# Performance work log

Measured on AMD Instinct MI355X. Metric: run time of the kernel, lower is better.

## Reference

```python
import jax, jax.numpy as jnp
import numpy as np

B, T, D, N, R, K = 4, 4096, 1024, 64, 16, 4  # batch, seq, d_model, state_size, dt_rank, conv_kernel


def setup_inputs() -> dict:
    key = jax.random.key(0)
    ks = jax.random.split(key, 6)
    s = 0.02  # small init scale (original uses xavier/zeros; random here for a meaningful baseline)
    return {
        "x": jax.random.normal(ks[0], (B, T, D), jnp.float32),
        "conv_w": jax.random.normal(ks[1], (D, K), jnp.float32) * s,  # depthwise conv kernel [D, K]
        "in_w": jax.random.normal(ks[2], (N, D), jnp.float32) * s,    # input_proj weight
        "in_b": jnp.zeros((N,), jnp.float32),
        "dt_w": jax.random.normal(ks[3], (R, D), jnp.float32) * s,    # delta_proj weight
        "dt_b": jnp.zeros((R,), jnp.float32),
        "tr_w": jax.random.normal(ks[4], (N, R), jnp.float32) * s,    # transition weight (no bias)
        "out_w": jax.random.normal(ks[5], (D, N), jnp.float32) * s,   # output_proj weight
        "out_b": jnp.zeros((D,), jnp.float32),
    }


def reference(x, conv_w, in_w, in_b, dt_w, dt_b, tr_w, out_w, out_b):
    Bx, Tx, Dx = x.shape
    k = conv_w.shape[1]
    # Causal depthwise conv: torch Conv1d(pad=k-1, groups=D) then slice [:T]
    xp = jnp.pad(x, ((0, 0), (k - 1, 0), (0, 0)))  # left-pad time axis
    conv_out = sum(xp[:, j:j + Tx, :] * conv_w[:, j] for j in range(k))  # [B,T,D]
    projected = (x + conv_out) @ in_w.T + in_b                 # [B,T,N]
    delta = jnp.tanh(x @ dt_w.T + dt_b) @ tr_w.T               # [B,T,N]

    def step(state, inp):
        d_t, p_t = inp  # each [B,N]
        state = jax.nn.silu(d_t + state) + p_t
        return state, state

    init = jnp.zeros((Bx, in_w.shape[0]), x.dtype)
    _, states = jax.lax.scan(step, init,
                             (jnp.swapaxes(delta, 0, 1), jnp.swapaxes(projected, 0, 1)))
    states = jnp.swapaxes(states, 0, 1)  # [B,T,N]
    return states @ out_w.T + out_b      # [B,T,D] (dropout=0.0 -> identity)
```

## Files before the change

kernel.cpp:

```cpp
#include <hip/hip_runtime.h>
#include <math.h>

#define Bn 4
#define Tn 4096
#define Dn 1024
#define Nn 64
#define Rn 16
#define KCONV 4

#define TT2 32
#define KCH 32
#define SU 32

typedef __attribute__((ext_vector_type(8))) short bf16x8;
typedef __attribute__((ext_vector_type(4))) float f32x4;

__device__ __forceinline__ unsigned short bf16_rne(float f) {
    unsigned int u = __float_as_uint(f);
    unsigned int r = (u + 0x7fffu + ((u >> 16) & 1u)) >> 16;
    return (unsigned short)r;
}


__global__ __launch_bounds__(128)
void prep_kernel(const float* __restrict__ x, const float* __restrict__ conv_w,
                 const float* __restrict__ in_w, const float* __restrict__ in_b,
                 const float* __restrict__ dt_w, const float* __restrict__ dt_b,
                 const float* __restrict__ tr_w,
                 float* __restrict__ O)
{
    __shared__ bf16x8 Axc_h[2][64], Axc_l[2][64];
    __shared__ bf16x8 Axr_h[2][64], Axr_l[2][64];
    __shared__ bf16x8 Bw_h[4][64],  Bw_l[4][64];
    __shared__ bf16x8 Bd_h[64],     Bd_l[64];
    __shared__ float  xs[35][36];
    __shared__ float4 cws[32];
    __shared__ float  AsS[TT2][17];
    __shared__ float  trS[Nn][17];

    const int tid = threadIdx.x;
    const int b   = blockIdx.y;
    const int t0  = blockIdx.x * TT2;
    const int l   = tid & 63;
    const int w   = tid >> 6;

    const float* xb = x + (size_t)b * Tn * Dn;

    for (int idx = tid; idx < Nn * Rn; idx += 128)
        trS[idx >> 4][idx & 15] = tr_w[idx];

    const f32x4 z4 = {0.f, 0.f, 0.f, 0.f};
    f32x4 accP[4] = {z4, z4, z4, z4};
    f32x4 accG = z4;

    for (int kc = 0; kc < Dn / KCH; ++kc) {
        const int k0 = kc * KCH;
        __syncthreads();

        {
            const int row  = tid >> 2;
            const int colg = tid & 3;
            const int tp   = t0 - 3 + row;
            float4 a = {0.f,0.f,0.f,0.f}, bq = {0.f,0.f,0.f,0.f};
            if (tp >= 0) {
                const float* src = &xb[(size_t)tp * Dn + k0 + 8 * colg];
                a  = *(const float4*)src;
                bq = *(const float4*)(src + 4);
            }
            *(float4*)&xs[row][8 * colg]     = a;
            *(float4*)&xs[row][8 * colg + 4] = bq;
            if (tid < 12) {
                const int row2 = 32 + (tid >> 2), colg2 = tid & 3;
                const float* s2 = &xb[(size_t)(t0 - 3 + row2) * Dn + k0 + 8 * colg2];
                *(float4*)&xs[row2][8 * colg2]     = *(const float4*)s2;
                *(float4*)&xs[row2][8 * colg2 + 4] = *(const float4*)(s2 + 4);
            }
            if (tid >= 64 && tid < 96)
                cws[tid - 64] = *(const float4*)&conv_w[(size_t)(k0 + tid - 64) * 4];
        }
        #pragma unroll
        for (int rep = 0; rep < 2; ++rep) {
            const int slot = tid + rep * 128;
            const int n = slot >> 2, s = slot & 3;
            const float* wp = &in_w[(size_t)n * Dn + k0 + 8 * s];
            float4 a  = *(const float4*)wp;
            float4 bq = *(const float4*)(wp + 4);
            float wv[8] = {a.x, a.y, a.z, a.w, bq.x, bq.y, bq.z, bq.w};
            bf16x8 fh, fl;
            #pragma unroll
            for (int k = 0; k < 8; ++k) {
                unsigned short h = bf16_rne(wv[k]);
                float hf = __uint_as_float((unsigned)h << 16);
                fh[k] = (short)h; fl[k] = (short)bf16_rne(wv[k] - hf);
            }
            Bw_h[n >> 4][(n & 15) | (s << 4)] = fh;
            Bw_l[n >> 4][(n & 15) | (s << 4)] = fl;
        }
        if (tid < 64) {
            const int r = tid >> 2, s = tid & 3;
            const float* wp = &dt_w[(size_t)r * Dn + k0 + 8 * s];
            float4 a  = *(const float4*)wp;
            float4 bq = *(const float4*)(wp + 4);
            float wv[8] = {a.x, a.y, a.z, a.w, bq.x, bq.y, bq.z, bq.w};
            bf16x8 fh, fl;
            #pragma unroll
            for (int k = 0; k < 8; ++k) {
                unsigned short h = bf16_rne(wv[k]);
                float hf = __uint_as_float((unsigned)h << 16);
                fh[k] = (short)h; fl[k] = (short)bf16_rne(wv[k] - hf);
            }
            Bd_h[r | (s << 4)] = fh; Bd_l[r | (s << 4)] = fl;
        }
        __syncthreads();

        {
            const int m = tid & 31;
            const int s = tid >> 5;
            float v[4][8];
            #pragma unroll
            for (int dr = 0; dr < 4; ++dr) {
                float4 a  = *(const float4*)&xs[m + dr][8 * s];
                float4 bq = *(const float4*)&xs[m + dr][8 * s + 4];
                v[dr][0]=a.x;  v[dr][1]=a.y;  v[dr][2]=a.z;  v[dr][3]=a.w;
                v[dr][4]=bq.x; v[dr][5]=bq.y; v[dr][6]=bq.z; v[dr][7]=bq.w;
            }
            bf16x8 fch, fcl, frh, frl;
            #pragma unroll
            for (int k = 0; k < 8; ++k) {
                float4 cw = cws[8 * s + k];
                float xr = v[3][k];
                float xc = xr;
                xc = fmaf(v[0][k], cw.x, xc);
                xc = fmaf(v[1][k], cw.y, xc);
                xc = fmaf(v[2][k], cw.z, xc);
                xc = fmaf(v[3][k], cw.w, xc);
                unsigned short h; float hf;
                h = bf16_rne(xc); hf = __uint_as_float((unsigned)h << 16);
                fch[k] = (short)h; fcl[k] = (short)bf16_rne(xc - hf);
                h = bf16_rne(xr); hf = __uint_as_float((unsigned)h << 16);
                frh[k] = (short)h; frl[k] = (short)bf16_rne(xr - hf);
            }
            const int lane = (m & 15) | (s << 4), mt = m >> 4;
            Axc_h[mt][lane] = fch; Axc_l[mt][lane] = fcl;
            Axr_h[mt][lane] = frh; Axr_l[mt][lane] = frl;
        }
        __syncthreads();

        bf16x8 axh = Axc_h[w][l], axl = Axc_l[w][l];
        bf16x8 arh = Axr_h[w][l], arl = Axr_l[w][l];
        #pragma unroll
        for (int nt = 0; nt < 4; ++nt) {
            bf16x8 bh = Bw_h[nt][l], bl = Bw_l[nt][l];
            accP[nt] = __builtin_amdgcn_mfma_f32_16x16x32_bf16(axh, bh, accP[nt], 0, 0, 0);
            accP[nt] = __builtin_amdgcn_mfma_f32_16x16x32_bf16(axl, bh, accP[nt], 0, 0, 0);
            accP[nt] = __builtin_amdgcn_mfma_f32_16x16x32_bf16(axh, bl, accP[nt], 0, 0, 0);
        }
        {
            bf16x8 bh = Bd_h[l], bl = Bd_l[l];
            accG = __builtin_amdgcn_mfma_f32_16x16x32_bf16(arh, bh, accG, 0, 0, 0);
            accG = __builtin_amdgcn_mfma_f32_16x16x32_bf16(arl, bh, accG, 0, 0, 0);
            accG = __builtin_amdgcn_mfma_f32_16x16x32_bf16(arh, bl, accG, 0, 0, 0);
        }
    }

    __syncthreads();
    #pragma unroll
    for (int i = 0; i < 4; ++i)
        AsS[16 * w + 4 * (l >> 4) + i][l & 15] = tanhf(accG[i] + dt_b[l & 15]);
    __syncthreads();

    float as_[4][16];
    #pragma unroll
    for (int i = 0; i < 4; ++i) {
        int mrow = 16 * w + 4 * (l >> 4) + i;
        #pragma unroll
        for (int j = 0; j < 4; ++j) {
            float4 q = *(const float4*)&AsS[mrow][4 * j];
            as_[i][4*j] = q.x; as_[i][4*j+1] = q.y;
            as_[i][4*j+2] = q.z; as_[i][4*j+3] = q.w;
        }
    }
    const int tile0 = t0 & ~63;
    const int coff  = t0 & 63;
    #pragma unroll
    for (int nt = 0; nt < 4; ++nt) {
        int n = 16 * nt + (l & 15);
        float tw[16];
        #pragma unroll
        for (int j = 0; j < 4; ++j) {
            float4 q = *(const float4*)&trS[n][4 * j];
            tw[4*j] = q.x; tw[4*j+1] = q.y; tw[4*j+2] = q.z; tw[4*j+3] = q.w;
        }
        float ib = in_b[n];
        #pragma unroll
        for (int i = 0; i < 4; ++i) {
            int mrow = 16 * w + 4 * (l >> 4) + i;
            float dlv = 0.f;
            #pragma unroll
            for (int r = 0; r < 16; ++r) dlv = fmaf(as_[i][r], tw[r], dlv);
            size_t a = ((size_t)(b * Tn + tile0 + n)) * Dn + coff + mrow;
            O[a]      = accP[nt][i] + ib;
            O[a + 64] = dlv;
        }
    }
}


typedef const __attribute__((address_space(1))) void GVoid;
typedef __attribute__((address_space(3))) void LVoid;
typedef __attribute__((address_space(3))) float LdsFloat;

#define WAITV(N) do {                                                    \
    asm volatile("s_waitcnt vmcnt(" #N ")" ::: "memory");                \
    __builtin_amdgcn_sched_barrier(0);                                   \
} while (0)

__device__ __forceinline__ void issue_chunk(float* lds, const float* rp)
{
    #pragma unroll
    for (int j = 0; j < 8; ++j)
        __builtin_amdgcn_global_load_lds((GVoid*)(rp + 4 * j),
                                         (LVoid*)(lds + j * 256), 16, 0, 0);
    #pragma unroll
    for (int j = 0; j < 8; ++j)
        __builtin_amdgcn_global_load_lds((GVoid*)(rp + 64 + 4 * j),
                                         (LVoid*)(lds + (8 + j) * 256), 16, 0, 0);
}

#define DS_READ_ALL(pv, dv, a)                                           \
    asm volatile(                                                        \
        "ds_read_b128 %0, %16 offset:0\n\t"                              \
        "ds_read_b128 %1, %16 offset:1024\n\t"                           \
        "ds_read_b128 %2, %16 offset:2048\n\t"                           \
        "ds_read_b128 %3, %16 offset:3072\n\t"                           \
        "ds_read_b128 %4, %16 offset:4096\n\t"                           \
        "ds_read_b128 %5, %16 offset:5120\n\t"                           \
        "ds_read_b128 %6, %16 offset:6144\n\t"                           \
        "ds_read_b128 %7, %16 offset:7168\n\t"                           \
        "ds_read_b128 %8, %16 offset:8192\n\t"                           \
        "ds_read_b128 %9, %16 offset:9216\n\t"                           \
        "ds_read_b128 %10, %16 offset:10240\n\t"                         \
        "ds_read_b128 %11, %16 offset:11264\n\t"                         \
        "ds_read_b128 %12, %16 offset:12288\n\t"                         \
        "ds_read_b128 %13, %16 offset:13312\n\t"                         \
        "ds_read_b128 %14, %16 offset:14336\n\t"                         \
        "ds_read_b128 %15, %16 offset:15360\n\t"                         \
        "s_waitcnt lgkmcnt(0)"                                           \
        : "=&v"(pv[0]), "=&v"(pv[1]), "=&v"(pv[2]), "=&v"(pv[3]),        \
          "=&v"(pv[4]), "=&v"(pv[5]), "=&v"(pv[6]), "=&v"(pv[7]),        \
          "=&v"(dv[0]), "=&v"(dv[1]), "=&v"(dv[2]), "=&v"(dv[3]),        \
          "=&v"(dv[4]), "=&v"(dv[5]), "=&v"(dv[6]), "=&v"(dv[7])         \
        : "v"(a) : "memory")

__device__ __forceinline__ void scan_chunk(const float* buf, int n, float& st,
                                           f32x4 (&sv)[8], float* sp)
{
    const float L2E = 1.44269504088896340736f;
    if (sp) {
        #pragma unroll
        for (int j = 0; j < 8; ++j)
            *(f32x4*)(sp + 4 * j) = sv[j];
    }
    unsigned a = (unsigned)(unsigned long long)(LdsFloat*)buf
               + (unsigned)(n * 16);
    f32x4 pv[8], dv[8];
    DS_READ_ALL(pv, dv, a);
    __builtin_amdgcn_sched_barrier(0);
    #pragma unroll
    for (int j = 0; j < 8; ++j) {
        #pragma unroll
        for (int i = 0; i < 4; ++i) {
            float d  = dv[j][i];
            float u  = st + d;
            float e  = __builtin_amdgcn_exp2f(fmaf(st, -L2E, -d * L2E));
            float r  = __builtin_amdgcn_rcpf(1.f + e);
            st = fmaf(u, r, pv[j][i]);
            sv[j][i] = st;
        }
    }
}

#define RP(c) (obase + (size_t)((((c) >> 1) * 64) + n) * Dn + ((c) & 1) * 32)
#define SP(c) (RP(c) + 128)

__global__ __launch_bounds__(64, 1)
void scan_kernel(float* __restrict__ O)
{
    __shared__ __align__(16) float buf[3][4096];

    const int b = blockIdx.x;
    const int n = threadIdx.x;
    float* obase = O + (size_t)b * Tn * Dn;

    float* b0 = buf[0];
    float* b1 = buf[1];
    float* b2 = buf[2];

    f32x4 sv[8];
    float st = 0.f;

    issue_chunk(b0, RP(0));
    issue_chunk(b1, RP(1));
    issue_chunk(b2, RP(2));
    WAITV(32);
    scan_chunk(b0, n, st, sv, nullptr);
    { float* t = b0; b0 = b1; b1 = b2; b2 = t; }

    issue_chunk(b2, RP(3));
    WAITV(32);
    scan_chunk(b0, n, st, sv, SP(0));
    { float* t = b0; b0 = b1; b1 = b2; b2 = t; }

    #pragma unroll 1
    for (int c = 2; c <= 125; ++c) {
        issue_chunk(b2, RP(c + 2));
        WAITV(40);
        scan_chunk(b0, n, st, sv, SP(c - 1));
        { float* t = b0; b0 = b1; b1 = b2; b2 = t; }
    }

    WAITV(24);
    scan_chunk(b0, n, st, sv, SP(125));
    { float* t = b0; b0 = b1; b1 = b2; b2 = t; }

    WAITV(16);
    scan_chunk(b0, n, st, sv, SP(126));

    {
        float* sp = SP(127);
        #pragma unroll
        for (int j = 0; j < 8; ++j)
            *(f32x4*)(sp + 4 * j) = sv[j];
    }
}

#undef RP
#undef SP

__global__ __launch_bounds__(256)
void out_kernel(const float* __restrict__ out_w, const float* __restrict__ out_b,
                float* __restrict__ O)
{
    __shared__ float Ss[64][Nn + 4];
    __shared__ float wT[Nn][64 + 4];

    const int tid = threadIdx.x;
    const int r0  = blockIdx.x * 64;
    const int c   = tid & 15;
    const int g   = tid >> 4;

    float4 wreg[4];
    #pragma unroll
    for (int q = 0; q < 4; ++q) {
        int idx = tid + q * 256;
        int dl = idx >> 4, n4 = (idx & 15) * 4;
        wreg[q] = *(const float4*)&out_w[(size_t)dl * Nn + n4];
    }

    for (int idx = tid; idx < 64 * 16; idx += 256) {
        int nn = idx >> 4, tg = idx & 15;
        float4 v = *(const float4*)&O[(size_t)(r0 + nn) * Dn + 128 + 4 * tg];
        Ss[4 * tg + 0][nn] = v.x;
        Ss[4 * tg + 1][nn] = v.y;
        Ss[4 * tg + 2][nn] = v.z;
        Ss[4 * tg + 3][nn] = v.w;
    }
    __syncthreads();

    for (int cb = 0; cb < Dn / 64; ++cb) {
        #pragma unroll
        for (int q = 0; q < 4; ++q) {
            int idx = tid + q * 256;
            int dl = idx >> 4, n4 = (idx & 15) * 4;
            wT[n4 + 0][dl] = wreg[q].x;
            wT[n4 + 1][dl] = wreg[q].y;
            wT[n4 + 2][dl] = wreg[q].z;
            wT[n4 + 3][dl] = wreg[q].w;
        }
        if (cb + 1 < Dn / 64) {
            const int d0n = (cb + 1) * 64;
            #pragma unroll
            for (int q = 0; q < 4; ++q) {
                int idx = tid + q * 256;
                int dl = idx >> 4, n4 = (idx & 15) * 4;
                wreg[q] = *(const float4*)&out_w[(size_t)(d0n + dl) * Nn + n4];
            }
        }
        __syncthreads();

        const int d0 = cb * 64;
        float acc[4][4] = {};
        #pragma unroll
        for (int kq = 0; kq < Nn; kq += 4) {
            float4 wv0 = *(const float4*)&wT[kq + 0][4 * c];
            float4 wv1 = *(const float4*)&wT[kq + 1][4 * c];
            float4 wv2 = *(const float4*)&wT[kq + 2][4 * c];
            float4 wv3 = *(const float4*)&wT[kq + 3][4 * c];
            #pragma unroll
            for (int i = 0; i < 4; ++i) {
                int row = g + 16 * i;
                float4 xv = *(const float4*)&Ss[row][kq];
                acc[i][0] = fmaf(xv.x, wv0.x, fmaf(xv.y, wv1.x, fmaf(xv.z, wv2.x, fmaf(xv.w, wv3.x, acc[i][0]))));
                acc[i][1] = fmaf(xv.x, wv0.y, fmaf(xv.y, wv1.y, fmaf(xv.z, wv2.y, fmaf(xv.w, wv3.y, acc[i][1]))));
                acc[i][2] = fmaf(xv.x, wv0.z, fmaf(xv.y, wv1.z, fmaf(xv.z, wv2.z, fmaf(xv.w, wv3.z, acc[i][2]))));
                acc[i][3] = fmaf(xv.x, wv0.w, fmaf(xv.y, wv1.w, fmaf(xv.z, wv2.w, fmaf(xv.w, wv3.w, acc[i][3]))));
            }
        }

        float4 bb = *(const float4*)&out_b[d0 + 4 * c];
        #pragma unroll
        for (int i = 0; i < 4; ++i) {
            int row = g + 16 * i;
            float4 o = make_float4(acc[i][0] + bb.x, acc[i][1] + bb.y,
                                   acc[i][2] + bb.z, acc[i][3] + bb.w);
            *(float4*)&O[(size_t)(r0 + row) * Dn + d0 + 4 * c] = o;
        }
        __syncthreads();
    }
}

extern "C" void kernel_launch(void* const* d_in, const int* in_sizes, int n_in,
                              void* d_out, int out_size, void* d_ws, size_t ws_size,
                              hipStream_t stream)
{
    const float* x      = (const float*)d_in[0];
    const float* conv_w = (const float*)d_in[1];
    const float* in_w   = (const float*)d_in[2];
    const float* in_b   = (const float*)d_in[3];
    const float* dt_w   = (const float*)d_in[4];
    const float* dt_b   = (const float*)d_in[5];
    const float* tr_w   = (const float*)d_in[6];
    const float* out_w  = (const float*)d_in[7];
    const float* out_b  = (const float*)d_in[8];
    float* O = (float*)d_out;
    (void)d_ws; (void)ws_size;

    dim3 g1(Tn / TT2, Bn);
    prep_kernel<<<g1, 128, 0, stream>>>(x, conv_w, in_w, in_b, dt_w, dt_b, tr_w, O);

    scan_kernel<<<dim3(Bn), 64, 0, stream>>>(O);

    out_kernel<<<dim3((Bn * Tn) / 64), 256, 0, stream>>>(out_w, out_b, O);
}
```

Before: 352.9 us.

## Precompute bf16 hi/lo weight splits in a separate kernel and DMA into LDS

Adds a small pre-kernel that converts in_w and dt_w into bf16 hi/lo MFMA-ready fragments once per call and stores them in workspace. The main prep kernel then streams those fragments directly into LDS with global_load_lds, replacing the per-block fp32 loads and split conversion that every one of the 512 blocks repeated. This trades redundant ALU and conversion work for one extra launch and a workspace round trip. The weight fragments in Bst now go straight from global memory to LDS and are read after the existing barriers, which rely on the vmcnt ordering of those DMA loads.

```diff
diff --git a/kernel.cpp b/kernel.cpp
--- a/kernel.cpp
+++ b/kernel.cpp
@@ -21,18 +21,65 @@
     return (unsigned short)r;
 }
 
+typedef const __attribute__((address_space(1))) void GVoid;
+typedef __attribute__((address_space(3))) void LVoid;
+typedef __attribute__((address_space(3))) float LdsFloat;
+
+
+__global__ __launch_bounds__(256)
+void prep0_kernel(const float* __restrict__ in_w, const float* __restrict__ dt_w,
+                  unsigned short* __restrict__ ws)
+{
+    const int kc  = blockIdx.x;
+    const int k0  = kc * KCH;
+    const int tid = threadIdx.x;
+    unsigned short* wsb = ws + (size_t)kc * 5120;
+
+    {
+        const int lane = tid & 63;
+        const int n = (tid >> 6) * 16 + (lane & 15), s = lane >> 4;
+        const float* wp = &in_w[(size_t)n * Dn + k0 + 8 * s];
+        float4 a  = *(const float4*)wp;
+        float4 bq = *(const float4*)(wp + 4);
+        float wv[8] = {a.x, a.y, a.z, a.w, bq.x, bq.y, bq.z, bq.w};
+        bf16x8 fh, fl;
+        #pragma unroll
+        for (int k = 0; k < 8; ++k) {
+            unsigned short h = bf16_rne(wv[k]);
+            float hf = __uint_as_float((unsigned)h << 16);
+            fh[k] = (short)h; fl[k] = (short)bf16_rne(wv[k] - hf);
+        }
+        *(bf16x8*)&wsb[(size_t)tid * 8]        = fh;
+        *(bf16x8*)&wsb[2048 + (size_t)tid * 8] = fl;
+    }
+    if (tid < 64) {
+        const int r = tid & 15, s = tid >> 4;
+        const float* wp = &dt_w[(size_t)r * Dn + k0 + 8 * s];
+        float4 a  = *(const float4*)wp;
+        float4 bq = *(const float4*)(wp + 4);
+        float wv[8] = {a.x, a.y, a.z, a.w, bq.x, bq.y, bq.z, bq.w};
+        bf16x8 fh, fl;
+        #pragma unroll
+        for (int k = 0; k < 8; ++k) {
+            unsigned short h = bf16_rne(wv[k]);
+            float hf = __uint_as_float((unsigned)h << 16);
+            fh[k] = (short)h; fl[k] = (short)bf16_rne(wv[k] - hf);
+        }
+        *(bf16x8*)&wsb[4096 + (size_t)tid * 8] = fh;
+        *(bf16x8*)&wsb[4608 + (size_t)tid * 8] = fl;
+    }
+}
 
 __global__ __launch_bounds__(128)
 void prep_kernel(const float* __restrict__ x, const float* __restrict__ conv_w,
-                 const float* __restrict__ in_w, const float* __restrict__ in_b,
-                 const float* __restrict__ dt_w, const float* __restrict__ dt_b,
+                 const unsigned short* __restrict__ ws,
+                 const float* __restrict__ in_b, const float* __restrict__ dt_b,
                  const float* __restrict__ tr_w,
                  float* __restrict__ O)
 {
     __shared__ bf16x8 Axc_h[2][64], Axc_l[2][64];
     __shared__ bf16x8 Axr_h[2][64], Axr_l[2][64];
-    __shared__ bf16x8 Bw_h[4][64],  Bw_l[4][64];
-    __shared__ bf16x8 Bd_h[64],     Bd_l[64];
+    __shared__ bf16x8 Bst[640];
     __shared__ float  xs[35][36];
     __shared__ float4 cws[32];
     __shared__ float  AsS[TT2][17];
@@ -56,6 +103,14 @@
     for (int kc = 0; kc < Dn / KCH; ++kc) {
         const int k0 = kc * KCH;
         __syncthreads();
+
+        if (tid < 64) {
+            const unsigned short* wsb = ws + (size_t)kc * 5120 + (size_t)l * 8;
+            #pragma unroll
+            for (int j = 0; j < 10; ++j)
+                __builtin_amdgcn_global_load_lds((GVoid*)(wsb + j * 512),
+                                                 (LVoid*)(Bst + j * 64), 16, 0, 0);
+        }
 
         {
             const int row  = tid >> 2;
@@ -77,39 +132,6 @@
             }
             if (tid >= 64 && tid < 96)
                 cws[tid - 64] = *(const float4*)&conv_w[(size_t)(k0 + tid - 64) * 4];
-        }
-        #pragma unroll
-        for (int rep = 0; rep < 2; ++rep) {
-            const int slot = tid + rep * 128;
-            const int n = slot >> 2, s = slot & 3;
-            const float* wp = &in_w[(size_t)n * Dn + k0 + 8 * s];
-            float4 a  = *(const float4*)wp;
-            float4 bq = *(const float4*)(wp + 4);
-            float wv[8] = {a.x, a.y, a.z, a.w, bq.x, bq.y, bq.z, bq.w};
-            bf16x8 fh, fl;
-            #pragma unroll
-            for (int k = 0; k < 8; ++k) {
-                unsigned short h = bf16_rne(wv[k]);
-                float hf = __uint_as_float((unsigned)h << 16);
-                fh[k] = (short)h; fl[k] = (short)bf16_rne(wv[k] - hf);
-            }
-            Bw_h[n >> 4][(n & 15) | (s << 4)] = fh;
-            Bw_l[n >> 4][(n & 15) | (s << 4)] = fl;
-        }
-        if (tid < 64) {
-            const int r = tid >> 2, s = tid & 3;
-            const float* wp = &dt_w[(size_t)r * Dn + k0 + 8 * s];
-            float4 a  = *(const float4*)wp;
-            float4 bq = *(const float4*)(wp + 4);
-            float wv[8] = {a.x, a.y, a.z, a.w, bq.x, bq.y, bq.z, bq.w};
-            bf16x8 fh, fl;
-            #pragma unroll
-            for (int k = 0; k < 8; ++k) {
-                unsigned short h = bf16_rne(wv[k]);
-                float hf = __uint_as_float((unsigned)h << 16);
-                fh[k] = (short)h; fl[k] = (short)bf16_rne(wv[k] - hf);
-            }
-            Bd_h[r | (s << 4)] = fh; Bd_l[r | (s << 4)] = fl;
         }
         __syncthreads();
 
@@ -150,13 +172,15 @@
         bf16x8 arh = Axr_h[w][l], arl = Axr_l[w][l];
         #pragma unroll
         for (int nt = 0; nt < 4; ++nt) {
-            bf16x8 bh = Bw_h[nt][l], bl = Bw_l[nt][l];
+            bf16x8 bh = Bst[nt * 64 + l];
+            bf16x8 bl = Bst[256 + nt * 64 + l];
             accP[nt] = __builtin_amdgcn_mfma_f32_16x16x32_bf16(axh, bh, accP[nt], 0, 0, 0);
             accP[nt] = __builtin_amdgcn_mfma_f32_16x16x32_bf16(axl, bh, accP[nt], 0, 0, 0);
             accP[nt] = __builtin_amdgcn_mfma_f32_16x16x32_bf16(axh, bl, accP[nt], 0, 0, 0);
         }
         {
-            bf16x8 bh = Bd_h[l], bl = Bd_l[l];
+            bf16x8 bh = Bst[512 + l];
+            bf16x8 bl = Bst[576 + l];
             accG = __builtin_amdgcn_mfma_f32_16x16x32_bf16(arh, bh, accG, 0, 0, 0);
             accG = __builtin_amdgcn_mfma_f32_16x16x32_bf16(arl, bh, accG, 0, 0, 0);
             accG = __builtin_amdgcn_mfma_f32_16x16x32_bf16(arh, bl, accG, 0, 0, 0);
@@ -205,10 +229,6 @@
     }
 }
 
-
-typedef const __attribute__((address_space(1))) void GVoid;
-typedef __attribute__((address_space(3))) void LVoid;
-typedef __attribute__((address_space(3))) float LdsFloat;
 
 #define WAITV(N) do {                                                    \
     asm volatile("s_waitcnt vmcnt(" #N ")" ::: "memory");                \
@@ -433,10 +453,13 @@
     const float* out_w  = (const float*)d_in[7];
     const float* out_b  = (const float*)d_in[8];
     float* O = (float*)d_out;
-    (void)d_ws; (void)ws_size;
+    unsigned short* ws = (unsigned short*)d_ws;
+    (void)ws_size;
+
+    prep0_kernel<<<dim3(Dn / KCH), 256, 0, stream>>>(in_w, dt_w, ws);
 
     dim3 g1(Tn / TT2, Bn);
-    prep_kernel<<<g1, 128, 0, stream>>>(x, conv_w, in_w, in_b, dt_w, dt_b, tr_w, O);
+    prep_kernel<<<g1, 128, 0, stream>>>(x, conv_w, ws, in_b, dt_b, tr_w, O);
 
     scan_kernel<<<dim3(Bn), 64, 0, stream>>>(O);
 
```

Result: faster. 337.4 us (-4.4%).
